# Kernel tuning notes

Hardware: AMD Instinct MI355X
Metric: run time of the kernel (lower is better)

Reference implementation:

```python
import jax, jax.numpy as jnp
import numpy as np


def setup_inputs() -> dict:
    key = jax.random.key(0)
    k1, k2, k3, k4 = jax.random.split(key, 4)
    B, h, w, z, C = 4, 16, 16, 16, 128
    Cq = C // 8
    x = jax.random.normal(k1, (B, h, w, z, C), dtype=jnp.float32)
    # 1x1x1 Conv3D kernels == per-voxel linear projections (he_normal scale)
    Wb = jax.random.normal(k2, (C, Cq), dtype=jnp.float32) * np.sqrt(2.0 / C)
    Wc = jax.random.normal(k3, (C, Cq), dtype=jnp.float32) * np.sqrt(2.0 / C)
    Wd = jax.random.normal(k4, (C, C), dtype=jnp.float32) * np.sqrt(2.0 / C)
    gamma = jnp.zeros((1,), dtype=jnp.float32)
    return {"x": x, "Wb": Wb, "Wc": Wc, "Wd": Wd, "gamma": gamma}


def reference(x, Wb, Wc, Wd, gamma):
    B, h, w, z, C = x.shape
    N = h * w * z
    # 1x1x1 convs = channel projections
    b = jnp.einsum('bhwzc,cf->bhwzf', x, Wb).reshape(B, N, -1)   # [B,N,C/8]
    c = jnp.einsum('bhwzc,cf->bhwzf', x, Wc).reshape(B, N, -1)   # [B,N,C/8]
    d = jnp.einsum('bhwzc,cf->bhwzf', x, Wd).reshape(B, N, C)    # [B,N,C]
    # full NxN attention scores, softmax over last axis (keras softmax default)
    scores = jnp.einsum('bnf,bmf->bnm', b, c)                    # [B,N,N]
    attn = jax.nn.softmax(scores, axis=-1)
    out = jnp.einsum('bnm,bmc->bnc', attn, d).reshape(B, h, w, z, C)
    return gamma * out + x
```

## Files before the change

### kernel.cpp

```cpp
#include <hip/hip_runtime.h>

#define NB     4
#define NN     4096
#define NC     128
#define NCQ    16
#define NROWS  (NB * NN)
#define NSLICE 8
#define NIT    (NN / 64 / NSLICE)

typedef __attribute__((ext_vector_type(8)))  __bf16 bf16x8;
typedef __attribute__((ext_vector_type(4)))  float  f32x4;
typedef __attribute__((ext_vector_type(16))) float  f32x16;

#define MFMA16(a,b,c) __builtin_amdgcn_mfma_f32_16x16x32_bf16((a),(b),(c),0,0,0)
#define MFMA32(a,b,c) __builtin_amdgcn_mfma_f32_32x32x16_bf16((a),(b),(c),0,0,0)
#define LOG2E 1.44269504f
#define SCH_BIAS 16248.66f

__device__ __forceinline__ f32x16 zero16() {
    f32x16 v;
    #pragma unroll
    for (int i = 0; i < 16; ++i) v[i] = 0.f;
    return v;
}


__global__ __launch_bounds__(256) void proj_kernel(
    const float* __restrict__ x,  const float* __restrict__ Wb,
    const float* __restrict__ Wc, const float* __restrict__ Wd,
    __bf16* __restrict__ qswz, __bf16* __restrict__ kswz,
    __bf16* __restrict__ vswz)
{
    __shared__ __align__(16) __bf16 xsh[32 * 136];
    __shared__ __align__(16) __bf16 wt [160 * 136];
    __shared__ __align__(16) float  osb[4][16 * 17];

    const int  t    = threadIdx.x;
    const int  lane = t & 63, w = t >> 6;
    const int  q16  = lane & 15, quad = lane >> 4;
    const long row0 = (long)blockIdx.x * 32;
    const int  batch = (int)(row0 >> 12);
    const int  nloc  = (int)(row0 & 4095);
    const int  rh   = w & 1;
    const int  og   = (w >> 1) * 5;

    #pragma unroll
    for (int i = 0; i < 4; ++i) {
        int idx = t + 256 * i;
        int r = idx >> 5, c4 = (idx & 31) * 4;
        float4 xv = *(const float4*)&x[(row0 + r) * NC + c4];
        union { __bf16 h[4]; uint2 u; } cv;
        cv.h[0] = (__bf16)xv.x; cv.h[1] = (__bf16)xv.y;
        cv.h[2] = (__bf16)xv.z; cv.h[3] = (__bf16)xv.w;
        *(uint2*)&xsh[r * 136 + c4] = cv.u;
    }
    #pragma unroll
    for (int i = 0; i < 2; ++i) {
        int idx = t + 256 * i;
        int ch = idx >> 2, o4 = (idx & 3) * 4;
        float4 v = *(const float4*)&Wb[ch * 16 + o4];
        wt[(o4 + 0) * 136 + ch] = (__bf16)v.x;
        wt[(o4 + 1) * 136 + ch] = (__bf16)v.y;
        wt[(o4 + 2) * 136 + ch] = (__bf16)v.z;
        wt[(o4 + 3) * 136 + ch] = (__bf16)v.w;
    }
    #pragma unroll
    for (int i = 0; i < 2; ++i) {
        int idx = t + 256 * i;
        int ch = idx >> 2, o4 = (idx & 3) * 4;
        float4 v = *(const float4*)&Wc[ch * 16 + o4];
        wt[(16 + o4 + 0) * 136 + ch] = (__bf16)v.x;
        wt[(16 + o4 + 1) * 136 + ch] = (__bf16)v.y;
        wt[(16 + o4 + 2) * 136 + ch] = (__bf16)v.z;
        wt[(16 + o4 + 3) * 136 + ch] = (__bf16)v.w;
    }
    #pragma unroll
    for (int i = 0; i < 16; ++i) {
        int idx = t + 256 * i;
        int ch = idx >> 5, o4 = (idx & 31) * 4;
        float4 v = *(const float4*)&Wd[ch * 128 + o4];
        wt[(32 + o4 + 0) * 136 + ch] = (__bf16)v.x;
        wt[(32 + o4 + 1) * 136 + ch] = (__bf16)v.y;
        wt[(32 + o4 + 2) * 136 + ch] = (__bf16)v.z;
        wt[(32 + o4 + 3) * 136 + ch] = (__bf16)v.w;
    }
    __syncthreads();

    bf16x8 xf[4];
    #pragma unroll
    for (int kc = 0; kc < 4; ++kc)
        xf[kc] = *(const bf16x8*)&xsh[(rh * 16 + q16) * 136 + kc * 32 + quad * 8];

    float* osw = osb[w];
    #pragma unroll
    for (int oc_t = 0; oc_t < 5; ++oc_t) {
        const int oset = og + oc_t;
        f32x4 acc = {0.f, 0.f, 0.f, 0.f};
        #pragma unroll
        for (int kc = 0; kc < 4; ++kc) {
            bf16x8 wf = *(const bf16x8*)&wt[(oset * 16 + q16) * 136 + kc * 32 + quad * 8];
            acc = MFMA16(wf, xf[kc], acc);
        }
        #pragma unroll
        for (int r = 0; r < 4; ++r)
            osw[(quad * 4 + r) * 17 + q16] = acc[r];

        if (oset >= 2) {
            int ch_l = lane & 15, lh_t = (lane >> 4) & 1, jh = lane >> 5;
            union { __bf16 h[4]; uint2 u; } cv;
            #pragma unroll
            for (int u2 = 0; u2 < 4; ++u2)
                cv.h[u2] = (__bf16)osw[ch_l * 17 + 8 * jh + 4 * lh_t + u2];
            int kb16 = (nloc >> 4) + rh;
            int cg   = (oset - 2) >> 1;
            int l31v = ((oset - 2) & 1) * 16 + ch_l;
            size_t off = ((((size_t)batch * 256 + kb16) * 4 + cg) << 9)
                       + (size_t)(lh_t * 32 + l31v) * 8 + jh * 4;
            *(uint2*)&vswz[off] = cv.u;
        } else if (lane < 32) {
            int xr = lane & 15, lh_t = lane >> 4;
            const float qsc = (oset == 0) ? LOG2E : 1.f;
            union { __bf16 h[8]; uint4 u; } cv;
            #pragma unroll
            for (int j = 0; j < 8; ++j)
                cv.h[j] = (__bf16)(osw[(8 * lh_t + j) * 17 + xr] * qsc);
            size_t off = ((((size_t)batch * 128 + (nloc >> 5)) * 64)
                       + (size_t)(lh_t * 32 + rh * 16 + xr)) * 8;
            __bf16* dst = (oset == 0) ? qswz : kswz;
            *(uint4*)&dst[off] = cv.u;
        }
    }
}

__global__ __launch_bounds__(256, 4) void attn_kernel(
    const __bf16* __restrict__ qswz, const __bf16* __restrict__ kswz,
    const __bf16* __restrict__ vswz, __bf16* __restrict__ Opart,
    float* __restrict__ lws)
{
    const int t    = threadIdx.x;
    const int lane = t & 63, w = t >> 6;
    const int l31 = lane & 31, lh = lane >> 5;
    const int bid   = blockIdx.x;
    const int xcd   = bid & 7;
    const int batch = xcd >> 1;
    const int spL   = xcd & 1;
    const int idx   = bid >> 3;
    const int qb32  = idx & 127;
    const int spH   = idx >> 7;
    const int h     = w & 1;
    const int slice = ((spH << 1) | spL) * 2 + (w >> 1);
    const int ks0   = slice * (64 * NIT);

    const bf16x8 qf = *(const bf16x8*)
        &qswz[(((size_t)batch * 128 + qb32) * 64 + lane) * 8];

    const __bf16* kptr = kswz + ((size_t)batch * 128 + (ks0 >> 5)) * 512 + lane * 8;
    const __bf16* vptr = vswz + ((size_t)batch * 256 + (ks0 >> 4)) * 2048
                       + h * 1024 + lane * 8;

    union { uint32_t u[4]; bf16x8 f; } onesu;
    #pragma unroll
    for (int i = 0; i < 4; ++i) onesu.u[i] = 0x3F803F80u;
    const bf16x8 ones = onesu.f;

    f32x16 O0 = zero16(), O1 = zero16(), Ol = zero16();

    bf16x8 kf0 = *(const bf16x8*)(kptr);
    bf16x8 kf1 = *(const bf16x8*)(kptr + 512);
    bf16x8 va[8], vb[8];
    #pragma unroll
    for (int b = 0; b < 4; ++b) {
        va[2*b]     = *(const bf16x8*)(vptr + (size_t)(b * 4)     * 512);
        va[2*b + 1] = *(const bf16x8*)(vptr + (size_t)(b * 4 + 1) * 512);
    }
    f32x16 S0 = MFMA32(kf0, qf, zero16());
    f32x16 S1 = MFMA32(kf1, qf, zero16());

#define ATTN_BODY(IT, CUR, NXT)                                               \
    {                                                                         \
        const int itn = ((IT) + 1 < NIT) ? (IT) + 1 : (IT);                   \
        kf0 = *(const bf16x8*)(kptr + (size_t)itn * 1024);                    \
        kf1 = *(const bf16x8*)(kptr + (size_t)itn * 1024 + 512);              \
        _Pragma("unroll")                                                     \
        for (int b = 0; b < 4; ++b) {                                         \
            NXT[2*b]     = *(const bf16x8*)(vptr + (size_t)((itn*4+b)*4)*512);\
            NXT[2*b + 1] = *(const bf16x8*)(vptr + (size_t)((itn*4+b)*4+1)*512);\
        }                                                                     \
        union { uint32_t u32[16]; bf16x8 f[4]; } pk;                          \
        _Pragma("unroll")                                                     \
        for (int i = 0; i < 8; ++i) {                                         \
            int e0 = (int)fmaf(S0[2*i],   128.f, SCH_BIAS);                   \
            int e1 = (int)fmaf(S0[2*i+1], 128.f, SCH_BIAS);                   \
            int e2 = (int)fmaf(S1[2*i],   128.f, SCH_BIAS);                   \
            int e3 = (int)fmaf(S1[2*i+1], 128.f, SCH_BIAS);                   \
            pk.u32[i]     = (uint32_t)((e1 << 16) | e0);                      \
            pk.u32[8 + i] = (uint32_t)((e3 << 16) | e2);                      \
        }                                                                     \
        _Pragma("unroll")                                                     \
        for (int b = 0; b < 4; ++b) {                                         \
            O0 = MFMA32(pk.f[b], CUR[2*b],     O0);                           \
            O1 = MFMA32(pk.f[b], CUR[2*b + 1], O1);                           \
            Ol = MFMA32(pk.f[b], ones,         Ol);                           \
        }                                                                     \
        S0 = MFMA32(kf0, qf, zero16());                                       \
        S1 = MFMA32(kf1, qf, zero16());                                       \
    }

    for (int it = 0; it < NIT; it += 2) {
        ATTN_BODY(it,     va, vb);
        ATTN_BODY(it + 1, vb, va);
    }
#undef ATTN_BODY

    const long base = (long)batch * NN;

    if (h == 0 && l31 == 0) {
        #pragma unroll
        for (int r = 0; r < 16; ++r) {
            int q = qb32 * 32 + (r & 3) + 8 * (r >> 2) + 4 * lh;
            lws[(size_t)slice * NROWS + base + q] = Ol[r];
        }
    }

    #pragma unroll
    for (int ct = 0; ct < 2; ++ct) {
        f32x16 Ov = ct ? O1 : O0;
        #pragma unroll
        for (int r = 0; r < 16; ++r) {
            int q = qb32 * 32 + (r & 3) + 8 * (r >> 2) + 4 * lh;
            Opart[((size_t)slice * NROWS + base + q) * NC + 64 * h + 32 * ct + l31]
                = (__bf16)Ov[r];
        }
    }
}

__global__ __launch_bounds__(256) void combine_kernel(
    const __bf16* __restrict__ Op, const float* __restrict__ lws,
    const float* __restrict__ x, const float* __restrict__ gamma,
    float* __restrict__ out)
{
    __shared__ float gl[32];
    const int  t    = threadIdx.x;
    const long row0 = (long)blockIdx.x * 32;
    if (t < 32) {
        float l = 0.f;
        #pragma unroll
        for (int s = 0; s < NSLICE; ++s) l += lws[(size_t)s * NROWS + row0 + t];
        gl[t] = gamma[0] / l;
    }
    __syncthreads();
    const size_t s1 = (size_t)NROWS * NC;
    #pragma unroll
    for (int i = 0; i < 4; ++i) {
        int idx = t + 256 * i;
        int r = idx >> 5, c4 = (idx & 31) * 4;
        size_t g = (size_t)(row0 + r) * NC + c4;
        float a0 = 0.f, a1 = 0.f, a2 = 0.f, a3 = 0.f;
        #pragma unroll
        for (int s = 0; s < NSLICE; ++s) {
            union { __bf16 h[4]; uint2 u; } a;
            a.u = *(const uint2*)&Op[s1 * s + g];
            a0 += (float)a.h[0]; a1 += (float)a.h[1];
            a2 += (float)a.h[2]; a3 += (float)a.h[3];
        }
        float sc = gl[r];
        float4 xv = *(const float4*)&x[g];
        float4 o;
        o.x = a0 * sc + xv.x; o.y = a1 * sc + xv.y;
        o.z = a2 * sc + xv.z; o.w = a3 * sc + xv.w;
        *(float4*)&out[g] = o;
    }
}

extern "C" void kernel_launch(void* const* d_in, const int* in_sizes, int n_in,
                              void* d_out, int out_size, void* d_ws, size_t ws_size,
                              hipStream_t stream) {
    const float* x     = (const float*)d_in[0];
    const float* Wb    = (const float*)d_in[1];
    const float* Wc    = (const float*)d_in[2];
    const float* Wd    = (const float*)d_in[3];
    const float* gamma = (const float*)d_in[4];
    float*       out   = (float*)d_out;

    __bf16* qswz  = (__bf16*)d_ws;
    __bf16* kswz  = qswz + (size_t)NROWS * NCQ;
    __bf16* vswz  = kswz + (size_t)NROWS * NCQ;
    __bf16* Opart = vswz + (size_t)NB * NC * NN;
    float*  lws   = (float*)(Opart + (size_t)NSLICE * NROWS * NC);

    proj_kernel   <<<NROWS / 32, 256, 0, stream>>>(x, Wb, Wc, Wd, qswz, kswz, vswz);
    attn_kernel   <<<NB * 128 * 2, 256, 0, stream>>>(qswz, kswz, vswz, Opart, lws);
    combine_kernel<<<NROWS / 32, 256, 0, stream>>>(Opart, lws, x, gamma, out);
}
```

Before: 107.8 us.

## Stage V tiles in shared memory and share them across four query blocks

Each block now holds four warps that handle four different 32-query blocks over the same key slice. V tiles are staged cooperatively into double-buffered LDS, so every wave computes all 128 output channels instead of half of them. Previously each wave loaded its own V fragments straight from global memory. The aim is to cut global and L2 traffic for V by reusing each tile across four query blocks. The cost is more LDS, a __syncthreads per iteration, more accumulator registers (occupancy lowered to 3) and duplicated score computation now gone while each wave does more PV MFMAs.

```diff
diff --git a/kernel.cpp b/kernel.cpp
--- a/kernel.cpp
+++ b/kernel.cpp
@@ -132,11 +132,13 @@
     }
 }
 
-__global__ __launch_bounds__(256, 4) void attn_kernel(
+__global__ __launch_bounds__(256, 3) void attn_kernel(
     const __bf16* __restrict__ qswz, const __bf16* __restrict__ kswz,
     const __bf16* __restrict__ vswz, __bf16* __restrict__ Opart,
     float* __restrict__ lws)
 {
+    __shared__ __align__(16) __bf16 vsh[2][8192];
+
     const int t    = threadIdx.x;
     const int lane = t & 63, w = t >> 6;
     const int l31 = lane & 31, lh = lane >> 5;
@@ -145,76 +147,85 @@
     const int batch = xcd >> 1;
     const int spL   = xcd & 1;
     const int idx   = bid >> 3;
-    const int qb32  = idx & 127;
-    const int spH   = idx >> 7;
-    const int h     = w & 1;
-    const int slice = ((spH << 1) | spL) * 2 + (w >> 1);
+    const int qq    = idx & 31;
+    const int spH   = idx >> 5;
+    const int slice = spH * 2 + spL;
+    const int qb32  = qq * 4 + w;
     const int ks0   = slice * (64 * NIT);
 
     const bf16x8 qf = *(const bf16x8*)
         &qswz[(((size_t)batch * 128 + qb32) * 64 + lane) * 8];
 
     const __bf16* kptr = kswz + ((size_t)batch * 128 + (ks0 >> 5)) * 512 + lane * 8;
-    const __bf16* vptr = vswz + ((size_t)batch * 256 + (ks0 >> 4)) * 2048
-                       + h * 1024 + lane * 8;
+    const __bf16* vsrc = vswz + ((size_t)batch * 256 + (ks0 >> 4)) * 2048;
 
     union { uint32_t u[4]; bf16x8 f; } onesu;
     #pragma unroll
     for (int i = 0; i < 4; ++i) onesu.u[i] = 0x3F803F80u;
     const bf16x8 ones = onesu.f;
 
-    f32x16 O0 = zero16(), O1 = zero16(), Ol = zero16();
-
+    f32x16 O0 = zero16(), O1 = zero16(), O2 = zero16(), O3 = zero16();
+    f32x16 Ol = zero16();
+
+    {
+        const uint4* src = (const uint4*)vsrc;
+        uint4*       dst = (uint4*)vsh[0];
+        #pragma unroll
+        for (int i = 0; i < 4; ++i) dst[t + 256 * i] = src[t + 256 * i];
+    }
     bf16x8 kf0 = *(const bf16x8*)(kptr);
     bf16x8 kf1 = *(const bf16x8*)(kptr + 512);
-    bf16x8 va[8], vb[8];
-    #pragma unroll
-    for (int b = 0; b < 4; ++b) {
-        va[2*b]     = *(const bf16x8*)(vptr + (size_t)(b * 4)     * 512);
-        va[2*b + 1] = *(const bf16x8*)(vptr + (size_t)(b * 4 + 1) * 512);
-    }
     f32x16 S0 = MFMA32(kf0, qf, zero16());
     f32x16 S1 = MFMA32(kf1, qf, zero16());
-
-#define ATTN_BODY(IT, CUR, NXT)                                               \
-    {                                                                         \
-        const int itn = ((IT) + 1 < NIT) ? (IT) + 1 : (IT);                   \
-        kf0 = *(const bf16x8*)(kptr + (size_t)itn * 1024);                    \
-        kf1 = *(const bf16x8*)(kptr + (size_t)itn * 1024 + 512);              \
-        _Pragma("unroll")                                                     \
-        for (int b = 0; b < 4; ++b) {                                         \
-            NXT[2*b]     = *(const bf16x8*)(vptr + (size_t)((itn*4+b)*4)*512);\
-            NXT[2*b + 1] = *(const bf16x8*)(vptr + (size_t)((itn*4+b)*4+1)*512);\
-        }                                                                     \
-        union { uint32_t u32[16]; bf16x8 f[4]; } pk;                          \
-        _Pragma("unroll")                                                     \
-        for (int i = 0; i < 8; ++i) {                                         \
-            int e0 = (int)fmaf(S0[2*i],   128.f, SCH_BIAS);                   \
-            int e1 = (int)fmaf(S0[2*i+1], 128.f, SCH_BIAS);                   \
-            int e2 = (int)fmaf(S1[2*i],   128.f, SCH_BIAS);                   \
-            int e3 = (int)fmaf(S1[2*i+1], 128.f, SCH_BIAS);                   \
-            pk.u32[i]     = (uint32_t)((e1 << 16) | e0);                      \
-            pk.u32[8 + i] = (uint32_t)((e3 << 16) | e2);                      \
-        }                                                                     \
-        _Pragma("unroll")                                                     \
-        for (int b = 0; b < 4; ++b) {                                         \
-            O0 = MFMA32(pk.f[b], CUR[2*b],     O0);                           \
-            O1 = MFMA32(pk.f[b], CUR[2*b + 1], O1);                           \
-            Ol = MFMA32(pk.f[b], ones,         Ol);                           \
-        }                                                                     \
-        S0 = MFMA32(kf0, qf, zero16());                                       \
-        S1 = MFMA32(kf1, qf, zero16());                                       \
-    }
-
-    for (int it = 0; it < NIT; it += 2) {
-        ATTN_BODY(it,     va, vb);
-        ATTN_BODY(it + 1, vb, va);
-    }
-#undef ATTN_BODY
+    __syncthreads();
+
+    for (int it = 0; it < NIT; ++it) {
+        const int buf = it & 1;
+        const int itn = (it + 1 < NIT) ? it + 1 : it;
+
+        kf0 = *(const bf16x8*)(kptr + (size_t)itn * 1024);
+        kf1 = *(const bf16x8*)(kptr + (size_t)itn * 1024 + 512);
+
+        {
+            const uint4* src = (const uint4*)(vsrc + (size_t)itn * 8192);
+            uint4*       dst = (uint4*)vsh[buf ^ 1];
+            #pragma unroll
+            for (int i = 0; i < 4; ++i) dst[t + 256 * i] = src[t + 256 * i];
+        }
+
+        union { uint32_t u32[16]; bf16x8 f[4]; } pk;
+        #pragma unroll
+        for (int i = 0; i < 8; ++i) {
+            int e0 = (int)fmaf(S0[2*i],   128.f, SCH_BIAS);
+            int e1 = (int)fmaf(S0[2*i+1], 128.f, SCH_BIAS);
+            int e2 = (int)fmaf(S1[2*i],   128.f, SCH_BIAS);
+            int e3 = (int)fmaf(S1[2*i+1], 128.f, SCH_BIAS);
+            pk.u32[i]     = (uint32_t)((e1 << 16) | e0);
+            pk.u32[8 + i] = (uint32_t)((e3 << 16) | e2);
+        }
+
+        #pragma unroll
+        for (int b = 0; b < 4; ++b) {
+            const __bf16* vr = &vsh[buf][b * 2048 + lane * 8];
+            bf16x8 v0 = *(const bf16x8*)(vr);
+            bf16x8 v1 = *(const bf16x8*)(vr + 512);
+            bf16x8 v2 = *(const bf16x8*)(vr + 1024);
+            bf16x8 v3 = *(const bf16x8*)(vr + 1536);
+            O0 = MFMA32(pk.f[b], v0, O0);
+            O1 = MFMA32(pk.f[b], v1, O1);
+            O2 = MFMA32(pk.f[b], v2, O2);
+            O3 = MFMA32(pk.f[b], v3, O3);
+            Ol = MFMA32(pk.f[b], ones, Ol);
+        }
+
+        S0 = MFMA32(kf0, qf, zero16());
+        S1 = MFMA32(kf1, qf, zero16());
+        __syncthreads();
+    }
 
     const long base = (long)batch * NN;
 
-    if (h == 0 && l31 == 0) {
+    if (l31 == 0) {
         #pragma unroll
         for (int r = 0; r < 16; ++r) {
             int q = qb32 * 32 + (r & 3) + 8 * (r >> 2) + 4 * lh;
@@ -223,12 +234,12 @@
     }
 
     #pragma unroll
-    for (int ct = 0; ct < 2; ++ct) {
-        f32x16 Ov = ct ? O1 : O0;
+    for (int cg = 0; cg < 4; ++cg) {
+        f32x16 Ov = (cg == 0) ? O0 : (cg == 1) ? O1 : (cg == 2) ? O2 : O3;
         #pragma unroll
         for (int r = 0; r < 16; ++r) {
             int q = qb32 * 32 + (r & 3) + 8 * (r >> 2) + 4 * lh;
-            Opart[((size_t)slice * NROWS + base + q) * NC + 64 * h + 32 * ct + l31]
+            Opart[((size_t)slice * NROWS + base + q) * NC + cg * 32 + l31]
                 = (__bf16)Ov[r];
         }
     }
@@ -289,6 +300,6 @@
     float*  lws   = (float*)(Opart + (size_t)NSLICE * NROWS * NC);
 
     proj_kernel   <<<NROWS / 32, 256, 0, stream>>>(x, Wb, Wc, Wd, qswz, kswz, vswz);
-    attn_kernel   <<<NB * 128 * 2, 256, 0, stream>>>(qswz, kswz, vswz, Opart, lws);
+    attn_kernel   <<<NB * 8 * 32, 256, 0, stream>>>(qswz, kswz, vswz, Opart, lws);
     combine_kernel<<<NROWS / 32, 256, 0, stream>>>(Opart, lws, x, gamma, out);
 }
```

Result: slower. 114.3 us (+6.0%).
